# Kernel tuning notes

Hardware: AMD Instinct MI355X
Metric: run time of the kernel (lower is better)

## Reference

```python
import jax, jax.numpy as jnp
import numpy as np

B, T, V, D, H, L = 256, 256, 128, 384, 6, 6
HS = D // H  # 64
FF = 4 * D


def _ln(x, g, b):
    m = jnp.mean(x, axis=-1, keepdims=True)
    v = jnp.var(x, axis=-1, keepdims=True)
    return (x - m) / jnp.sqrt(v + 1e-5) * g + b


def setup_inputs() -> dict:
    key = jax.random.key(0)
    ks = jax.random.split(key, 16)
    s = lambda k, sh: jax.random.normal(k, sh, dtype=jnp.float32) * 0.02
    return {
        "idx": jax.random.randint(ks[0], (B, T), 0, V),
        "tok_emb": s(ks[1], (V, D)),
        "pos_emb": s(ks[2], (T, D)),
        "Wq": s(ks[3], (L, H, D, HS)),
        "Wk": s(ks[4], (L, H, D, HS)),
        "Wv": s(ks[5], (L, H, D, HS)),
        "Wproj": s(ks[6], (L, D, D)),
        "bproj": jnp.zeros((L, D), jnp.float32),
        "ln1_g": jnp.ones((L, D), jnp.float32),
        "ln1_b": jnp.zeros((L, D), jnp.float32),
        "ln2_g": jnp.ones((L, D), jnp.float32),
        "ln2_b": jnp.zeros((L, D), jnp.float32),
        "W1": s(ks[7], (L, D, FF)),
        "b1": jnp.zeros((L, FF), jnp.float32),
        "W2": s(ks[8], (L, FF, D)),
        "b2": jnp.zeros((L, D), jnp.float32),
        "lnf_g": jnp.ones((D,), jnp.float32),
        "lnf_b": jnp.zeros((D,), jnp.float32),
        "Wlm": s(ks[9], (D, V)),
        "blm": jnp.zeros((V,), jnp.float32),
    }


def reference(idx, tok_emb, pos_emb, Wq, Wk, Wv, Wproj, bproj,
              ln1_g, ln1_b, ln2_g, ln2_b, W1, b1, W2, b2,
              lnf_g, lnf_b, Wlm, blm):
    Bv, Tv = idx.shape
    x = tok_emb[idx] + pos_emb[:Tv]  # [B,T,D]
    mask = jnp.tril(jnp.ones((Tv, Tv), dtype=bool))
    scale = HS ** -0.5
    for l in range(L):
        xn = _ln(x, ln1_g[l], ln1_b[l])
        q = jnp.einsum('btd,hdk->bhtk', xn, Wq[l])
        k = jnp.einsum('btd,hdk->bhtk', xn, Wk[l])
        v = jnp.einsum('btd,hdk->bhtk', xn, Wv[l])
        wei = jnp.einsum('bhtk,bhsk->bhts', q, k) * scale  # [B,H,T,T]
        wei = jnp.where(mask, wei, -jnp.inf)
        wei = jax.nn.softmax(wei, axis=-1)
        o = jnp.einsum('bhts,bhsk->bhtk', wei, v)
        o = o.transpose(0, 2, 1, 3).reshape(Bv, Tv, D)  # concat heads
        x = x + o @ Wproj[l] + bproj[l]
        xn = _ln(x, ln2_g[l], ln2_b[l])
        x = x + jax.nn.relu(xn @ W1[l] + b1[l]) @ W2[l] + b2[l]
    x = _ln(x, lnf_g, lnf_b)
    return x @ Wlm + blm  # logits [B,T,V]
```

## Files before the change

### kernel.cpp

```cpp
#include <hip/hip_runtime.h>
#include <stdint.h>

typedef unsigned short u16;
typedef __attribute__((ext_vector_type(8))) short short8;
typedef __attribute__((ext_vector_type(4))) float floatx4;

#define BB 256
#define TT 256
#define VOC 128
#define DD 384
#define HH 6
#define LLAY 6
#define HS 64
#define FFF 1536
#define BT (BB*TT)

__device__ __forceinline__ float b2f(u16 u) {
  union { float f; uint32_t i; } x; x.i = ((uint32_t)u) << 16; return x.f;
}
__device__ __forceinline__ u16 f2b(float f) {
  union { float f; uint32_t i; } x; x.f = f;
  uint32_t r = x.i + 0x7fffu + ((x.i >> 16) & 1u);
  return (u16)(r >> 16);
}
__device__ __forceinline__ float ldf(const void* p, size_t i, int bf) {
  return bf ? b2f(((const u16*)p)[i]) : ((const float*)p)[i];
}
__device__ __forceinline__ int get_bf(const u16* probe) {
  return probe[0] == 0x3F80;
}

__device__ __forceinline__ void gl2lds16(const u16* g, u16* l) {
  __builtin_amdgcn_global_load_lds(
      (const __attribute__((address_space(1))) unsigned int*)g,
      (__attribute__((address_space(3))) unsigned int*)l, 16, 0, 0);
}

__global__ __launch_bounds__(256) void k_repack_qkv(
    const void* __restrict__ Wq, const void* __restrict__ Wk,
    const void* __restrict__ Wv, u16* __restrict__ out,
    const void* __restrict__ g1, const void* __restrict__ b1n,
    float* __restrict__ u, float* __restrict__ v, const u16* probe) {
  __shared__ float t[32][33];
  int bf = get_bf(probe);
  int z = blockIdx.z;
  int h = z % 6, ls = z / 6, sel = ls % 3, l = ls / 3;
  const void* W = sel == 0 ? Wq : (sel == 1 ? Wk : Wv);
  int c0 = blockIdx.x * 32;
  int r0 = blockIdx.y * 32;
  int tx = threadIdx.x & 31, ty = threadIdx.x >> 5;
#pragma unroll
  for (int i = 0; i < 32; i += 8)
    t[ty + i][tx] = ldf(W, (((size_t)(l * 6 + h)) * 384 + r0 + ty + i) * 64 + c0 + tx, bf);
  __syncthreads();
  float gv = ldf(g1, (size_t)l * 384 + r0 + tx, bf);
  float bv = ldf(b1n, (size_t)l * 384 + r0 + tx, bf);
#pragma unroll
  for (int i = 0; i < 32; i += 8) {
    float w = t[tx][ty + i];
    int n = sel * 384 + h * 64 + c0 + ty + i;
    out[((size_t)l * 1152 + n) * 384 + r0 + tx] = f2b(w * gv);
    float pu = w * gv, pv = w * bv;
#pragma unroll
    for (int m = 1; m < 32; m <<= 1) { pu += __shfl_xor(pu, m); pv += __shfl_xor(pv, m); }
    if (tx == 0) {
      atomicAdd(&u[(size_t)l * 1152 + n], pu);
      atomicAdd(&v[(size_t)l * 1152 + n], pv);
    }
  }
}

__global__ __launch_bounds__(256) void k_transpose(
    const void* __restrict__ in, u16* __restrict__ out, int R, int C,
    const u16* probe) {
  __shared__ float t[32][33];
  int bf = get_bf(probe);
  int c0 = blockIdx.x * 32, r0 = blockIdx.y * 32, l = blockIdx.z;
  int tx = threadIdx.x & 31, ty = threadIdx.x >> 5;
  size_t base = (size_t)l * R * C;
#pragma unroll
  for (int i = 0; i < 32; i += 8)
    t[ty + i][tx] = ldf(in, base + (size_t)(r0 + ty + i) * C + c0 + tx, bf);
  __syncthreads();
#pragma unroll
  for (int i = 0; i < 32; i += 8)
    out[base + (size_t)(c0 + ty + i) * R + r0 + tx] = f2b(t[tx][ty + i]);
}

__global__ __launch_bounds__(256) void k_transpose_ln(
    const void* __restrict__ in, u16* __restrict__ out, int R, int C,
    const void* __restrict__ g, const void* __restrict__ b,
    float* __restrict__ u, float* __restrict__ v, const u16* probe) {
  __shared__ float t[32][33];
  int bf = get_bf(probe);
  int c0 = blockIdx.x * 32, r0 = blockIdx.y * 32, l = blockIdx.z;
  int tx = threadIdx.x & 31, ty = threadIdx.x >> 5;
  size_t base = (size_t)l * R * C;
#pragma unroll
  for (int i = 0; i < 32; i += 8)
    t[ty + i][tx] = ldf(in, base + (size_t)(r0 + ty + i) * C + c0 + tx, bf);
  __syncthreads();
  float gv = ldf(g, (size_t)l * R + r0 + tx, bf);
  float bv = ldf(b, (size_t)l * R + r0 + tx, bf);
#pragma unroll
  for (int i = 0; i < 32; i += 8) {
    float w = t[tx][ty + i];
    out[base + (size_t)(c0 + ty + i) * R + r0 + tx] = f2b(w * gv);
    float pu = w * gv, pv = w * bv;
#pragma unroll
    for (int m = 1; m < 32; m <<= 1) { pu += __shfl_xor(pu, m); pv += __shfl_xor(pv, m); }
    if (tx == 0) {
      atomicAdd(&u[(size_t)l * C + c0 + ty + i], pu);
      atomicAdd(&v[(size_t)l * C + c0 + ty + i], pv);
    }
  }
}

__global__ __launch_bounds__(256) void k_embed(
    const int* __restrict__ idx, const void* __restrict__ tok,
    const void* __restrict__ pos, u16* __restrict__ X,
    float* __restrict__ stp, const u16* probe) {
  int bf = get_bf(probe);
  int gw = (blockIdx.x * 256 + threadIdx.x) >> 6;
  int lane = threadIdx.x & 63;
  int nw = (gridDim.x * 256) >> 6;
  for (int row = gw; row < BT; row += nw) {
    int v = idx[row];
    size_t tb = (size_t)v * DD, pb = (size_t)(row & 255) * DD;
    u16* xr = X + (size_t)row * DD;
    float s = 0.f, ss = 0.f;
#pragma unroll
    for (int i = 0; i < 6; ++i) {
      int d = i * 64 + lane;
      float x = ldf(tok, tb + d, bf) + ldf(pos, pb + d, bf);
      u16 xb = f2b(x);
      xr[d] = xb;
      float v2 = b2f(xb);
      s += v2; ss += v2 * v2;
    }
#pragma unroll
    for (int m = 1; m < 64; m <<= 1) { s += __shfl_xor(s, m); ss += __shfl_xor(ss, m); }
    if (lane < 6) {
      float2 pr;
      pr.x = (lane == 0) ? s : 0.f;
      pr.y = (lane == 0) ? ss : 0.f;
      *(float2*)(stp + (size_t)row * 12 + lane * 2) = pr;
    }
  }
}

template <int EPI>
__global__ __launch_bounds__(512) void k_gemm(
    const u16* __restrict__ A, const u16* __restrict__ Bt,
    const void* __restrict__ bias, int boff, u16* __restrict__ Xb,
    u16* __restrict__ C, float* __restrict__ Cf, int N, int K,
    const float* __restrict__ u, const float* __restrict__ v,
    float* __restrict__ stp, const u16* probe) {
  __shared__ u16 As[256 * 64];
  __shared__ u16 Bs[128 * 64];
  __shared__ float stl[256][2];
  int tid = threadIdx.x, lane = tid & 63, wave = tid >> 6;
  int m0 = blockIdx.x * 256, n0 = blockIdx.y * 128;

  if (EPI != 2) {
    if (tid < 256) {
      const float* p = stp + (size_t)(m0 + tid) * 12;
      float s = 0.f, ss = 0.f;
#pragma unroll
      for (int k2 = 0; k2 < 6; ++k2) { s += p[2 * k2]; ss += p[2 * k2 + 1]; }
      float mean = s * (1.f / DD);
      float var = ss * (1.f / DD) - mean * mean;
      stl[tid][0] = mean;
      stl[tid][1] = rsqrtf(var + 1e-5f);
    }
  }

  int srow = tid >> 3;
  int skg = ((tid & 7) ^ (srow & 7)) * 8;
  const u16* gA = A + (size_t)(m0 + srow) * K + skg;
  const u16* gB = Bt + (size_t)(n0 + srow) * K + skg;
  u16* lA = As + wave * 512;
  u16* lB = Bs + wave * 512;
  int wy = wave >> 1, wx = wave & 1;
  int lr = lane & 15, quad = lane >> 4;
  int sx = lr & 7;
  floatx4 acc[4][4];
#pragma unroll
  for (int i = 0; i < 4; ++i)
#pragma unroll
    for (int j = 0; j < 4; ++j) acc[i][j] = (floatx4){0.f, 0.f, 0.f, 0.f};

  const u16* Abase = As + (size_t)(wy * 64 + lr) * 64;
  const u16* Bbase = Bs + (size_t)(wx * 64 + lr) * 64;

  int nk = K >> 6;
  for (int bk = 0; bk < nk; ++bk) {
    __syncthreads();
#pragma unroll
    for (int c = 0; c < 4; ++c)
      gl2lds16(gA + (size_t)(c * 64) * K, lA + c * 4096);
#pragma unroll
    for (int c = 0; c < 2; ++c)
      gl2lds16(gB + (size_t)(c * 64) * K, lB + c * 4096);
    gA += 64; gB += 64;
    __syncthreads();
#pragma unroll
    for (int half = 0; half < 2; ++half) {
      int ko = ((quad + half * 4) ^ sx) * 8;
      short8 af[4], bfr[4];
#pragma unroll
      for (int i = 0; i < 4; ++i) af[i] = *(const short8*)(Abase + i * 1024 + ko);
#pragma unroll
      for (int j = 0; j < 4; ++j) bfr[j] = *(const short8*)(Bbase + j * 1024 + ko);
#pragma unroll
      for (int i = 0; i < 4; ++i)
#pragma unroll
        for (int j = 0; j < 4; ++j)
          acc[i][j] = __builtin_amdgcn_mfma_f32_16x16x32_bf16(af[i], bfr[j], acc[i][j], 0, 0, 0);
    }
  }

  if (EPI == 2) {
    int bfl = get_bf(probe);
    float bv2[4];
#pragma unroll
    for (int j = 0; j < 4; ++j)
      bv2[j] = ldf(bias, boff + n0 + wx * 64 + j * 16 + lr, bfl);
    int slot = blockIdx.y * 2 + wx;
#pragma unroll
    for (int i = 0; i < 4; ++i) {
      int mrow = m0 + wy * 64 + i * 16 + quad * 4;
#pragma unroll
      for (int r = 0; r < 4; ++r) {
        int grow = mrow + r;
        float s = 0.f, ss = 0.f;
#pragma unroll
        for (int j = 0; j < 4; ++j) {
          int n = n0 + wx * 64 + j * 16 + lr;
          size_t off = (size_t)grow * N + n;
          u16 val = f2b(b2f(Xb[off]) + acc[i][j][r] + bv2[j]);
          Xb[off] = val;
          float yr = b2f(val);
          s += yr; ss += yr * yr;
        }
#pragma unroll
        for (int m = 1; m < 16; m <<= 1) { s += __shfl_xor(s, m); ss += __shfl_xor(ss, m); }
        if (lr == 0) {
          float2 pr; pr.x = s; pr.y = ss;
          *(float2*)(stp + ((size_t)grow * 6 + slot) * 2) = pr;
        }
      }
    }
  } else {
    int bfl = (EPI == 1 || EPI == 3) ? get_bf(probe) : 1;
    float un[4], vn[4], bv[4], sc[4];
    size_t sb[4]; int nc[4];
#pragma unroll
    for (int j = 0; j < 4; ++j) {
      int n = n0 + wx * 64 + j * 16 + lr;
      un[j] = u[n]; vn[j] = v[n];
      bv[j] = (EPI == 4) ? 0.f : ldf(bias, boff + n, bfl);
      sc[j] = 1.f;
      if (EPI == 4) {
        int sel = n >= 768 ? 2 : (n >= 384 ? 1 : 0);
        int hh = (n - sel * 384) >> 6;
        sb[j] = (size_t)sel * boff * 384 + (size_t)hh * boff * 64;
        nc[j] = n & 63;
        if (sel == 0) sc[j] = 0.125f;
      }
    }
#pragma unroll
    for (int i = 0; i < 4; ++i) {
      int lrow0 = wy * 64 + i * 16 + quad * 4;
#pragma unroll
      for (int r = 0; r < 4; ++r) {
        int lrow = lrow0 + r;
        int grow = m0 + lrow;
        float mu = stl[lrow][0], rs = stl[lrow][1];
#pragma unroll
        for (int j = 0; j < 4; ++j) {
          int n = n0 + wx * 64 + j * 16 + lr;
          float y = rs * (acc[i][j][r] - mu * un[j]) + vn[j];
          if (EPI == 1) C[(size_t)grow * N + n] = f2b(fmaxf(y + bv[j], 0.f));
          else if (EPI == 3) {
            if (bfl) C[(size_t)grow * N + n] = f2b(y + bv[j]);
            else Cf[(size_t)grow * N + n] = y + bv[j];
          } else {
            C[sb[j] + (size_t)grow * 64 + nc[j]] = f2b(y * sc[j]);
          }
        }
      }
    }
  }
}

__global__ __launch_bounds__(256) void k_attn(
    const u16* __restrict__ Q, const u16* __restrict__ K,
    const u16* __restrict__ V, u16* __restrict__ O, int TB) {
  __shared__ u16 Vt[2][64 * 72];
  __shared__ u16 P[4 * 16 * 72];
  int bx = blockIdx.x;
  int h = blockIdx.y;
  int b = blockIdx.z;
  int tid = threadIdx.x, lane = tid & 63, wave = tid >> 6;
  int lr = lane & 15, quad = lane >> 4;
  size_t hbase = (size_t)h * TB;
  const u16* Vb = V + (hbase + b * TT) * 64;

  int sp = tid & 31, sc = tid >> 5;

  {
    const u16* v0 = Vb + (size_t)(2 * sp) * 64 + sc * 8;
    short8 a = *(const short8*)(v0);
    short8 bvv = *(const short8*)(v0 + 64);
#pragma unroll
    for (int e = 0; e < 8; ++e) {
      uint32_t pk = (uint32_t)(u16)a[e] | ((uint32_t)(u16)bvv[e] << 16);
      *(uint32_t*)&Vt[0][(sc * 8 + e) * 72 + 2 * sp] = pk;
    }
  }

  int t0w = bx * 64 + wave * 16;
  const u16* qrow = Q + (hbase + b * TT + t0w + lr) * 64 + quad * 8;
  short8 qf0 = *(const short8*)(qrow);
  short8 qf1 = *(const short8*)(qrow + 32);

  const u16* kbase0 = K + (hbase + b * TT + lr) * 64 + quad * 8;
  short8 kc[8];
#pragma unroll
  for (int cc = 0; cc < 4; ++cc) {
    kc[2 * cc]     = *(const short8*)(kbase0 + cc * 16 * 64);
    kc[2 * cc + 1] = *(const short8*)(kbase0 + cc * 16 * 64 + 32);
  }

  float ls[4];
  floatx4 oacc[4];
#pragma unroll
  for (int r = 0; r < 4; ++r) ls[r] = 0.f;
#pragma unroll
  for (int j2 = 0; j2 < 4; ++j2) oacc[j2] = (floatx4){0.f, 0.f, 0.f, 0.f};
  u16* Pw = P + wave * 1152;
  const u16* Pr = P + wave * 1152 + lr * 72 + quad * 8;

  __syncthreads();

  for (int ks = 0; ks <= bx; ++ks) {
    short8 kn[8], sva, svb;
    bool do_stage = (ks < bx);
    if (do_stage) {
      const u16* kb2 = kbase0 + (size_t)(ks + 1) * 64 * 64;
#pragma unroll
      for (int cc = 0; cc < 4; ++cc) {
        kn[2 * cc]     = *(const short8*)(kb2 + cc * 16 * 64);
        kn[2 * cc + 1] = *(const short8*)(kb2 + cc * 16 * 64 + 32);
      }
      const u16* v0 = Vb + (size_t)((ks + 1) * 64 + 2 * sp) * 64 + sc * 8;
      sva = *(const short8*)(v0);
      svb = *(const short8*)(v0 + 64);
    }

    floatx4 s[4];
#pragma unroll
    for (int cc = 0; cc < 4; ++cc) s[cc] = (floatx4){0.f, 0.f, 0.f, 0.f};
#pragma unroll
    for (int cc = 0; cc < 4; ++cc) {
      s[cc] = __builtin_amdgcn_mfma_f32_16x16x32_bf16(qf0, kc[2 * cc], s[cc], 0, 0, 0);
      s[cc] = __builtin_amdgcn_mfma_f32_16x16x32_bf16(qf1, kc[2 * cc + 1], s[cc], 0, 0, 0);
    }

    if (ks == bx) {
#pragma unroll
      for (int r = 0; r < 4; ++r) {
        int rowt = t0w + quad * 4 + r;
#pragma unroll
        for (int cc = 0; cc < 4; ++cc) {
          int c = ks * 64 + cc * 16 + lr;
          float e = (c > rowt) ? 0.f : __expf(s[cc][r]);
          ls[r] += e;
          Pw[(quad * 4 + r) * 72 + cc * 16 + lr] = f2b(e);
        }
      }
    } else {
#pragma unroll
      for (int r = 0; r < 4; ++r)
#pragma unroll
        for (int cc = 0; cc < 4; ++cc) {
          float e = __expf(s[cc][r]);
          ls[r] += e;
          Pw[(quad * 4 + r) * 72 + cc * 16 + lr] = f2b(e);
        }
    }
    asm volatile("s_waitcnt lgkmcnt(0)" ::: "memory");
    const u16* Vc = &Vt[ks & 1][0];
#pragma unroll
    for (int h2 = 0; h2 < 2; ++h2) {
      short8 pf = *(const short8*)(Pr + h2 * 32);
#pragma unroll
      for (int j2 = 0; j2 < 4; ++j2) {
        short8 vf = *(const short8*)(Vc + (j2 * 16 + lr) * 72 + h2 * 32 + quad * 8);
        oacc[j2] = __builtin_amdgcn_mfma_f32_16x16x32_bf16(pf, vf, oacc[j2], 0, 0, 0);
      }
    }

    if (do_stage) {
      u16* dst = &Vt[(ks + 1) & 1][0];
#pragma unroll
      for (int e = 0; e < 8; ++e) {
        uint32_t pk = (uint32_t)(u16)sva[e] | ((uint32_t)(u16)svb[e] << 16);
        *(uint32_t*)&dst[(sc * 8 + e) * 72 + 2 * sp] = pk;
      }
#pragma unroll
      for (int e = 0; e < 8; ++e) kc[e] = kn[e];
    }
    __syncthreads();
  }

#pragma unroll
  for (int r = 0; r < 4; ++r) {
#pragma unroll
    for (int mm = 1; mm < 16; mm <<= 1) ls[r] += __shfl_xor(ls[r], mm);
    ls[r] = 1.f / ls[r];
  }

  u16* Ot = (u16*)Vt;
#pragma unroll
  for (int j2 = 0; j2 < 4; ++j2)
#pragma unroll
    for (int r = 0; r < 4; ++r)
      Ot[(wave * 16 + quad * 4 + r) * 72 + j2 * 16 + lr] = f2b(oacc[j2][r] * ls[r]);
  __syncthreads();
#pragma unroll
  for (int p = 0; p < 2; ++p) {
    int row = p * 32 + (tid >> 3), cg = tid & 7;
    short8 o8 = *(const short8*)(Ot + row * 72 + cg * 8);
    *(short8*)(O + (size_t)(b * TT + bx * 64 + row) * DD + h * 64 + cg * 8) = o8;
  }
}

extern "C" void kernel_launch(void* const* d_in, const int* in_sizes, int n_in,
                              void* d_out, int out_size, void* d_ws, size_t ws_size,
                              hipStream_t stream) {
  const int* idx   = (const int*)d_in[0];
  const void* tok  = d_in[1];
  const void* pos  = d_in[2];
  const void* Wq   = d_in[3];
  const void* Wk   = d_in[4];
  const void* Wv   = d_in[5];
  const void* Wproj= d_in[6];
  const void* bproj= d_in[7];
  const void* ln1g = d_in[8];
  const void* ln1b = d_in[9];
  const void* ln2g = d_in[10];
  const void* ln2b = d_in[11];
  const void* W1   = d_in[12];
  const void* b1   = d_in[13];
  const void* W2   = d_in[14];
  const void* b2   = d_in[15];
  const void* lnfg = d_in[16];
  const void* lnfb = d_in[17];
  const void* Wlm  = d_in[18];
  const void* blm  = d_in[19];
  const u16* probe = (const u16*)d_in[8];

  char* ws = (char*)d_ws;
  u16* X  = (u16*)ws;
  u16* XA = (u16*)(ws + 50331648);
  char* wb = ws + 100663296;
  u16* Wqkv_t  = (u16*)wb;
  u16* Wproj_t = (u16*)(wb + 5308416);
  u16* W1_t    = (u16*)(wb + 7077888);
  u16* W2_t    = (u16*)(wb + 14155776);
  u16* Wlm_t   = (u16*)(wb + 21233664);
  char* uvb = wb + 21331968;
  float* u_qkv = (float*)uvb;
  float* v_qkv = (float*)(uvb + 27648);
  float* u_fc1 = (float*)(uvb + 55296);
  float* v_fc1 = (float*)(uvb + 92160);
  float* u_lm  = (float*)(uvb + 129024);
  float* v_lm  = (float*)(uvb + 129536);
  float* stp   = (float*)(uvb + 130048 + 524288);
  const size_t fixed = 100663296 + 21331968 + 130048 + 524288 + 3145728;
  u16* S  = (u16*)(ws + fixed);

  size_t avail = ws_size > fixed ? ws_size - fixed : 0;
  int nA = 8, nM = 8;
  if ((size_t)BT * 1152 * 2 <= avail) nA = 1;
  else if ((size_t)(BT / 2) * 1152 * 2 <= avail) nA = 2;
  else if ((size_t)(BT / 4) * 1152 * 2 <= avail) nA = 4;
  if ((size_t)BT * 1536 * 2 <= avail) nM = 1;
  else if ((size_t)(BT / 2) * 1536 * 2 <= avail) nM = 2;
  else if ((size_t)(BT / 4) * 1536 * 2 <= avail) nM = 4;
  const int rowsA = BT / nA;
  const int rowsM = BT / nM;

  hipMemsetAsync(uvb, 0, 130048, stream);
  { dim3 g(2, 12, 108);
    k_repack_qkv<<<g, 256, 0, stream>>>(Wq, Wk, Wv, Wqkv_t, ln1g, ln1b,
                                        u_qkv, v_qkv, probe); }
  { dim3 g(12, 12, 6);   k_transpose<<<g, 256, 0, stream>>>(Wproj, Wproj_t, 384, 384, probe); }
  { dim3 g(48, 12, 6);
    k_transpose_ln<<<g, 256, 0, stream>>>(W1, W1_t, 384, 1536, ln2g, ln2b,
                                          u_fc1, v_fc1, probe); }
  { dim3 g(12, 48, 6);   k_transpose<<<g, 256, 0, stream>>>(W2, W2_t, 1536, 384, probe); }
  { dim3 g(4, 12, 1);
    k_transpose_ln<<<g, 256, 0, stream>>>(Wlm, Wlm_t, 384, 128, lnfg, lnfb,
                                          u_lm, v_lm, probe); }

  k_embed<<<2048, 256, 0, stream>>>(idx, tok, pos, X, stp, probe);

  for (int l = 0; l < LLAY; ++l) {
    for (int c = 0; c < nA; ++c) {
      const u16* A0c = X + (size_t)c * rowsA * DD;
      { dim3 g(rowsA / 256, 9);
        k_gemm<4><<<g, 512, 0, stream>>>(A0c, Wqkv_t + (size_t)l * 1152 * 384,
                                         nullptr, rowsA, nullptr, S, nullptr, 1152, 384,
                                         u_qkv + l * 1152, v_qkv + l * 1152,
                                         stp + (size_t)c * rowsA * 12, probe); }
      { dim3 g(4, HH, rowsA / 256);
        k_attn<<<g, 256, 0, stream>>>(S, S + (size_t)6 * rowsA * 64,
                                      S + (size_t)12 * rowsA * 64,
                                      XA + (size_t)c * rowsA * DD, rowsA); }
    }
    { dim3 g(256, 3);
      k_gemm<2><<<g, 512, 0, stream>>>(XA, Wproj_t + (size_t)l * 384 * 384,
                                       bproj, l * 384, X, nullptr, nullptr, 384, 384,
                                       nullptr, nullptr, stp, probe); }
    for (int c = 0; c < nM; ++c) {
      const u16* A0c = X + (size_t)c * rowsM * DD;
      { dim3 g(rowsM / 256, 12);
        k_gemm<1><<<g, 512, 0, stream>>>(A0c, W1_t + (size_t)l * 1536 * 384,
                                         b1, l * 1536, nullptr, S, nullptr, 1536, 384,
                                         u_fc1 + l * 1536, v_fc1 + l * 1536,
                                         stp + (size_t)c * rowsM * 12, probe); }
      { dim3 g(rowsM / 256, 3);
        k_gemm<2><<<g, 512, 0, stream>>>(S, W2_t + (size_t)l * 384 * 1536,
                                         b2, l * 384, X + (size_t)c * rowsM * DD,
                                         nullptr, nullptr, 384, 1536,
                                         nullptr, nullptr,
                                         stp + (size_t)c * rowsM * 12, probe); }
    }
  }
  { dim3 g(256, 1);
    k_gemm<3><<<g, 512, 0, stream>>>(X, Wlm_t, blm, 0, nullptr,
                                     (u16*)d_out, (float*)d_out, 128, 384,
                                     u_lm, v_lm, stp, probe); }
}
```

Before: 3.108 ms.

## Restructure attention to one block per (head,batch) with full V in LDS

The attention kernel now launches one 512-thread block per head and sequence instead of four 256-thread blocks per query chunk. The whole transposed V for the sequence is staged once in LDS. Each wave handles two 16-row query tiles, reading K fragments straight from global memory, with no per-step double buffering or block barriers. This removes redundant V staging across query-chunk blocks and the per-iteration __syncthreads. In exchange the causal work is unevenly spread across waves, K loads are no longer prefetched, and fewer blocks are launched.

Result: faster. 2.708 ms (-12.8%).

```diff
diff --git a/kernel.cpp b/kernel.cpp
--- a/kernel.cpp
+++ b/kernel.cpp
@@ -294,146 +294,126 @@
   }
 }
 
-__global__ __launch_bounds__(256) void k_attn(
+__global__ __launch_bounds__(512, 6) void k_attn(
     const u16* __restrict__ Q, const u16* __restrict__ K,
     const u16* __restrict__ V, u16* __restrict__ O, int TB) {
-  __shared__ u16 Vt[2][64 * 72];
-  __shared__ u16 P[4 * 16 * 72];
-  int bx = blockIdx.x;
-  int h = blockIdx.y;
-  int b = blockIdx.z;
+  __shared__ u16 Vt[64 * 264];
+  __shared__ u16 P[8][16 * 72];
+  int h = blockIdx.x;
+  int b = blockIdx.y;
   int tid = threadIdx.x, lane = tid & 63, wave = tid >> 6;
   int lr = lane & 15, quad = lane >> 4;
   size_t hbase = (size_t)h * TB;
   const u16* Vb = V + (hbase + b * TT) * 64;
-
-  int sp = tid & 31, sc = tid >> 5;
+  const u16* Kb = K + (hbase + b * TT) * 64;
+  const u16* Qb = Q + (hbase + b * TT) * 64;
 
   {
-    const u16* v0 = Vb + (size_t)(2 * sp) * 64 + sc * 8;
-    short8 a = *(const short8*)(v0);
-    short8 bvv = *(const short8*)(v0 + 64);
+    int rp = tid & 127, oc2 = tid >> 7;
+    const u16* v0 = Vb + (size_t)(2 * rp) * 64 + oc2 * 16;
+    short8 a0 = *(const short8*)(v0);
+    short8 a1 = *(const short8*)(v0 + 8);
+    short8 b0 = *(const short8*)(v0 + 64);
+    short8 b1 = *(const short8*)(v0 + 72);
 #pragma unroll
     for (int e = 0; e < 8; ++e) {
-      uint32_t pk = (uint32_t)(u16)a[e] | ((uint32_t)(u16)bvv[e] << 16);
-      *(uint32_t*)&Vt[0][(sc * 8 + e) * 72 + 2 * sp] = pk;
-    }
-  }
-
-  int t0w = bx * 64 + wave * 16;
-  const u16* qrow = Q + (hbase + b * TT + t0w + lr) * 64 + quad * 8;
-  short8 qf0 = *(const short8*)(qrow);
-  short8 qf1 = *(const short8*)(qrow + 32);
-
-  const u16* kbase0 = K + (hbase + b * TT + lr) * 64 + quad * 8;
-  short8 kc[8];
-#pragma unroll
-  for (int cc = 0; cc < 4; ++cc) {
-    kc[2 * cc]     = *(const short8*)(kbase0 + cc * 16 * 64);
-    kc[2 * cc + 1] = *(const short8*)(kbase0 + cc * 16 * 64 + 32);
-  }
-
-  float ls[4];
-  floatx4 oacc[4];
-#pragma unroll
-  for (int r = 0; r < 4; ++r) ls[r] = 0.f;
-#pragma unroll
-  for (int j2 = 0; j2 < 4; ++j2) oacc[j2] = (floatx4){0.f, 0.f, 0.f, 0.f};
-  u16* Pw = P + wave * 1152;
-  const u16* Pr = P + wave * 1152 + lr * 72 + quad * 8;
-
+      int d0 = oc2 * 16 + e, d1 = d0 + 8;
+      uint32_t p0 = (uint32_t)(u16)a0[e] | ((uint32_t)(u16)b0[e] << 16);
+      uint32_t p1 = (uint32_t)(u16)a1[e] | ((uint32_t)(u16)b1[e] << 16);
+      *(uint32_t*)&Vt[d0 * 264 + 2 * rp] = p0;
+      *(uint32_t*)&Vt[d1 * 264 + 2 * rp] = p1;
+    }
+  }
   __syncthreads();
 
-  for (int ks = 0; ks <= bx; ++ks) {
-    short8 kn[8], sva, svb;
-    bool do_stage = (ks < bx);
-    if (do_stage) {
-      const u16* kb2 = kbase0 + (size_t)(ks + 1) * 64 * 64;
+  u16* Pw = P[wave];
+  const u16* Pr = Pw + lr * 72 + quad * 8;
+
+#pragma unroll
+  for (int tt = 0; tt < 2; ++tt) {
+    int t = wave * 2 + tt;
+    int r0 = t * 16;
+    const u16* qrow = Qb + (size_t)(r0 + lr) * 64 + quad * 8;
+    short8 qf0 = *(const short8*)(qrow);
+    short8 qf1 = *(const short8*)(qrow + 32);
+    int nk = (t >> 2) + 1;
+
+    float ls[4];
+    floatx4 oacc[4];
+#pragma unroll
+    for (int r = 0; r < 4; ++r) ls[r] = 0.f;
+#pragma unroll
+    for (int j2 = 0; j2 < 4; ++j2) oacc[j2] = (floatx4){0.f, 0.f, 0.f, 0.f};
+
+    for (int ks = 0; ks < nk; ++ks) {
+      floatx4 s[4];
+#pragma unroll
+      for (int cc = 0; cc < 4; ++cc) s[cc] = (floatx4){0.f, 0.f, 0.f, 0.f};
+      const u16* kbase = Kb + (size_t)(ks * 64 + lr) * 64 + quad * 8;
 #pragma unroll
       for (int cc = 0; cc < 4; ++cc) {
-        kn[2 * cc]     = *(const short8*)(kb2 + cc * 16 * 64);
-        kn[2 * cc + 1] = *(const short8*)(kb2 + cc * 16 * 64 + 32);
+        const u16* kr = kbase + cc * 16 * 64;
+        short8 kf;
+        kf = *(const short8*)(kr);      s[cc] = __builtin_amdgcn_mfma_f32_16x16x32_bf16(qf0, kf, s[cc], 0, 0, 0);
+        kf = *(const short8*)(kr + 32); s[cc] = __builtin_amdgcn_mfma_f32_16x16x32_bf16(qf1, kf, s[cc], 0, 0, 0);
       }
-      const u16* v0 = Vb + (size_t)((ks + 1) * 64 + 2 * sp) * 64 + sc * 8;
-      sva = *(const short8*)(v0);
-      svb = *(const short8*)(v0 + 64);
-    }
-
-    floatx4 s[4];
-#pragma unroll
-    for (int cc = 0; cc < 4; ++cc) s[cc] = (floatx4){0.f, 0.f, 0.f, 0.f};
-#pragma unroll
-    for (int cc = 0; cc < 4; ++cc) {
-      s[cc] = __builtin_amdgcn_mfma_f32_16x16x32_bf16(qf0, kc[2 * cc], s[cc], 0, 0, 0);
-      s[cc] = __builtin_amdgcn_mfma_f32_16x16x32_bf16(qf1, kc[2 * cc + 1], s[cc], 0, 0, 0);
-    }
-
-    if (ks == bx) {
-#pragma unroll
-      for (int r = 0; r < 4; ++r) {
-        int rowt = t0w + quad * 4 + r;
-#pragma unroll
-        for (int cc = 0; cc < 4; ++cc) {
-          int c = ks * 64 + cc * 16 + lr;
-          float e = (c > rowt) ? 0.f : __expf(s[cc][r]);
-          ls[r] += e;
-          Pw[(quad * 4 + r) * 72 + cc * 16 + lr] = f2b(e);
+
+      if (ks == nk - 1) {
+#pragma unroll
+        for (int r = 0; r < 4; ++r) {
+          int rowt = r0 + quad * 4 + r;
+#pragma unroll
+          for (int cc = 0; cc < 4; ++cc) {
+            int c = ks * 64 + cc * 16 + lr;
+            float e = (c > rowt) ? 0.f : __expf(s[cc][r]);
+            ls[r] += e;
+            Pw[(quad * 4 + r) * 72 + cc * 16 + lr] = f2b(e);
+          }
+        }
+      } else {
+#pragma unroll
+        for (int r = 0; r < 4; ++r)
+#pragma unroll
+          for (int cc = 0; cc < 4; ++cc) {
+            float e = __expf(s[cc][r]);
+            ls[r] += e;
+            Pw[(quad * 4 + r) * 72 + cc * 16 + lr] = f2b(e);
+          }
+      }
+      asm volatile("s_waitcnt lgkmcnt(0)" ::: "memory");
+#pragma unroll
+      for (int h2 = 0; h2 < 2; ++h2) {
+        short8 pf = *(const short8*)(Pr + h2 * 32);
+#pragma unroll
+        for (int j2 = 0; j2 < 4; ++j2) {
+          short8 vf = *(const short8*)(Vt + (j2 * 16 + lr) * 264 + ks * 64 + h2 * 32 + quad * 8);
+          oacc[j2] = __builtin_amdgcn_mfma_f32_16x16x32_bf16(pf, vf, oacc[j2], 0, 0, 0);
         }
       }
-    } else {
+    }
+
+#pragma unroll
+    for (int r = 0; r < 4; ++r) {
+#pragma unroll
+      for (int mm = 1; mm < 16; mm <<= 1) ls[r] += __shfl_xor(ls[r], mm);
+      ls[r] = 1.f / ls[r];
+    }
+
+    asm volatile("s_waitcnt lgkmcnt(0)" ::: "memory");
+#pragma unroll
+    for (int j2 = 0; j2 < 4; ++j2)
 #pragma unroll
       for (int r = 0; r < 4; ++r)
-#pragma unroll
-        for (int cc = 0; cc < 4; ++cc) {
-          float e = __expf(s[cc][r]);
-          ls[r] += e;
-          Pw[(quad * 4 + r) * 72 + cc * 16 + lr] = f2b(e);
-        }
-    }
+        Pw[(quad * 4 + r) * 72 + j2 * 16 + lr] = f2b(oacc[j2][r] * ls[r]);
     asm volatile("s_waitcnt lgkmcnt(0)" ::: "memory");
-    const u16* Vc = &Vt[ks & 1][0];
-#pragma unroll
-    for (int h2 = 0; h2 < 2; ++h2) {
-      short8 pf = *(const short8*)(Pr + h2 * 32);
-#pragma unroll
-      for (int j2 = 0; j2 < 4; ++j2) {
-        short8 vf = *(const short8*)(Vc + (j2 * 16 + lr) * 72 + h2 * 32 + quad * 8);
-        oacc[j2] = __builtin_amdgcn_mfma_f32_16x16x32_bf16(pf, vf, oacc[j2], 0, 0, 0);
-      }
-    }
-
-    if (do_stage) {
-      u16* dst = &Vt[(ks + 1) & 1][0];
-#pragma unroll
-      for (int e = 0; e < 8; ++e) {
-        uint32_t pk = (uint32_t)(u16)sva[e] | ((uint32_t)(u16)svb[e] << 16);
-        *(uint32_t*)&dst[(sc * 8 + e) * 72 + 2 * sp] = pk;
-      }
-#pragma unroll
-      for (int e = 0; e < 8; ++e) kc[e] = kn[e];
-    }
-    __syncthreads();
-  }
-
-#pragma unroll
-  for (int r = 0; r < 4; ++r) {
-#pragma unroll
-    for (int mm = 1; mm < 16; mm <<= 1) ls[r] += __shfl_xor(ls[r], mm);
-    ls[r] = 1.f / ls[r];
-  }
-
-  u16* Ot = (u16*)Vt;
-#pragma unroll
-  for (int j2 = 0; j2 < 4; ++j2)
-#pragma unroll
-    for (int r = 0; r < 4; ++r)
-      Ot[(wave * 16 + quad * 4 + r) * 72 + j2 * 16 + lr] = f2b(oacc[j2][r] * ls[r]);
-  __syncthreads();
-#pragma unroll
-  for (int p = 0; p < 2; ++p) {
-    int row = p * 32 + (tid >> 3), cg = tid & 7;
-    short8 o8 = *(const short8*)(Ot + row * 72 + cg * 8);
-    *(short8*)(O + (size_t)(b * TT + bx * 64 + row) * DD + h * 64 + cg * 8) = o8;
+#pragma unroll
+    for (int p = 0; p < 2; ++p) {
+      int idx = p * 64 + lane;
+      int row = idx >> 3, cg = idx & 7;
+      short8 o8 = *(const short8*)(Pw + row * 72 + cg * 8);
+      *(short8*)(O + (size_t)(b * TT + r0 + row) * DD + h * 64 + cg * 8) = o8;
+    }
+    asm volatile("s_waitcnt lgkmcnt(0) vmcnt(0)" ::: "memory");
   }
 }
 
@@ -516,8 +496,8 @@
                                          nullptr, rowsA, nullptr, S, nullptr, 1152, 384,
                                          u_qkv + l * 1152, v_qkv + l * 1152,
                                          stp + (size_t)c * rowsA * 12, probe); }
-      { dim3 g(4, HH, rowsA / 256);
-        k_attn<<<g, 256, 0, stream>>>(S, S + (size_t)6 * rowsA * 64,
+      { dim3 g(HH, rowsA / TT);
+        k_attn<<<g, 512, 0, stream>>>(S, S + (size_t)6 * rowsA * 64,
                                       S + (size_t)12 * rowsA * 64,
                                       XA + (size_t)c * rowsA * DD, rowsA); }
     }
```
